# Optimization experiments

Hardware: AMD Instinct MI355X
Metric: run time of the kernel (lower is better)

The kernel has to match this reference:

```python
import jax, jax.numpy as jnp
import numpy as np

N = 1_000_000  # nodes
E = 1_000_000  # edges (== N so poss_edge can be indexed by node ids AND edge masks, as in source)
C = 64         # classes; poss_edge has C+1 columns (last = 'intrust')
SEMI_LAMBDA = 0.5
EDGE_LAMBDA = 1.0


def setup_inputs() -> dict:
    key = jax.random.key(0)
    k1, k2, k3, k4, k5 = jax.random.split(key, 5)
    # probabilities strictly positive so log() is finite
    poss_node = jax.random.uniform(k1, (N, C), jnp.float32, 0.05, 1.0)
    poss_edge = jax.random.uniform(k2, (E, C + 1), jnp.float32, 0.05, 1.0)
    groundTruth = jax.random.randint(k3, (N,), 0, C)
    mask = jax.random.randint(k4, (N,), 0, 2).astype(bool)
    edges = jax.random.randint(k5, (E, 2), 0, N)
    return {"poss_node": poss_node, "poss_edge": poss_edge,
            "groundTruth": groundTruth, "mask": mask, "edges": edges}


def reference(poss_node, poss_edge, groundTruth, mask, edges):
    dt = poss_node.dtype
    maskf = mask.astype(dt)
    # --- node NLL loss: mean of -log p[i, gt[i]] over masked nodes ---
    logp = jnp.log(poss_node[jnp.arange(N), groundTruth])  # [N]
    loss = -jnp.sum(maskf * logp) / jnp.sum(maskf)

    e0, e1 = edges[:, 0], edges[:, 1]
    intrust = jax.lax.stop_gradient(poss_edge[:, -1])  # detach

    # --- semi loss (faithful to source: scalar sq-diff times sum(1-intrust)) ---
    if SEMI_LAMBDA >= 1e-9:
        sqdiff = jnp.sum((poss_edge[e0] - poss_edge[e1]) ** 2)  # scalar
        semi_loss = SEMI_LAMBDA * jnp.sum(1.0 - intrust) * sqdiff
    else:
        semi_loss = jnp.zeros((), dt)

    # --- edge label splits ---
    m0, m1 = mask[e0], mask[e1]
    label_mask = m0 | m1
    both = m0 & m1
    gt0, gt1 = groundTruth[e0], groundTruth[e1]
    same = both & (gt0 == gt1)
    diff = both & (gt0 != gt1)
    single = label_mask & ~both
    left_s = single & m0
    right_s = single & m1

    rows = jnp.arange(E)
    p_gt0 = poss_edge[rows, gt0]   # [E] prob of left node's label
    p_gt1 = poss_edge[rows, gt1]   # [E] prob of right node's label
    p_last = poss_edge[:, -1]      # [E] 'no-edge' / intrust column

    z = jnp.zeros((), dt)
    raw = (-jnp.sum(jnp.where(same, jnp.log(p_gt0), z))
           - jnp.sum(jnp.where(diff, jnp.log(p_last), z))
           - jnp.sum(jnp.where(left_s, jnp.log(p_last + p_gt0), z))
           - jnp.sum(jnp.where(right_s, jnp.log(p_last + p_gt1), z)))
    S = jnp.sum(label_mask.astype(dt))
    # source applies (*= edge_lambda; /= S) twice
    edge_loss = raw * (EDGE_LAMBDA * EDGE_LAMBDA) / (S * S)

    return loss + semi_loss + edge_loss
```

## Files before the change

### kernel.cpp

```cpp
#include <hip/hip_runtime.h>
#include <math.h>

namespace {
constexpr int N = 1000000;
constexpr int E = 1000000;
constexpr int C = 64;
constexpr int NODE_BLOCKS = 1024;
constexpr int EDGE_BLOCKS = 2048;
constexpr int BLOCK = 256;
constexpr int GROUPS_PER_BLOCK = BLOCK / 16;
constexpr int TOTAL_GROUPS = EDGE_BLOCKS * GROUPS_PER_BLOCK;
constexpr double SEMI_LAMBDA = 0.5;
constexpr double EDGE_LAMBDA = 1.0;
}

__device__ __forceinline__ float waveReduceSum(float v) {
#pragma unroll
    for (int off = 32; off > 0; off >>= 1) v += __shfl_down(v, off, 64);
    return v;
}

__global__ __launch_bounds__(BLOCK) void node_kernel(
    const float* __restrict__ poss_node,
    const int* __restrict__ gt,
    const int* __restrict__ mask,
    float* __restrict__ partials)
{
    float lsum = 0.f, cnt = 0.f;
    for (int i = blockIdx.x * BLOCK + threadIdx.x; i < N; i += NODE_BLOCKS * BLOCK) {
        if (mask[i] != 0) {
            lsum += logf(poss_node[(size_t)i * C + gt[i]]);
            cnt += 1.f;
        }
    }
    __shared__ float s0[BLOCK / 64], s1[BLOCK / 64];
    lsum = waveReduceSum(lsum);
    cnt  = waveReduceSum(cnt);
    const int lane = threadIdx.x & 63, wv = threadIdx.x >> 6;
    if (lane == 0) { s0[wv] = lsum; s1[wv] = cnt; }
    __syncthreads();
    if (threadIdx.x == 0) {
        float a = 0.f, b = 0.f;
#pragma unroll
        for (int w = 0; w < BLOCK / 64; ++w) { a += s0[w]; b += s1[w]; }
        partials[blockIdx.x]               = a;
        partials[NODE_BLOCKS + blockIdx.x] = b;
    }
}

__global__ __launch_bounds__(BLOCK) void edge_kernel(
    const float* __restrict__ poss_edge,
    const int* __restrict__ gt,
    const int* __restrict__ mask,
    const int* __restrict__ edges,
    float* __restrict__ partials)
{
    const int t   = threadIdx.x & 15;
    const int grp = threadIdx.x >> 4;
    const int globalGroup = blockIdx.x * GROUPS_PER_BLOCK + grp;

    float s1 = 0.f, sq = 0.f, pos = 0.f, lcnt = 0.f;

    for (int e = globalGroup; e < E; e += TOTAL_GROUPS) {
        const int2 ep = *(const int2*)(edges + 2 * (size_t)e);
        const int e0 = ep.x, e1 = ep.y;

        const float* __restrict__ ra = poss_edge + (size_t)e0 * (C + 1);
        const float* __restrict__ rb = poss_edge + (size_t)e1 * (C + 1);
        const float* __restrict__ re = poss_edge + (size_t)e  * (C + 1);

        const float a0 = ra[t], a1 = ra[t + 16], a2 = ra[t + 32], a3 = ra[t + 48];
        const float b0 = rb[t], b1 = rb[t + 16], b2 = rb[t + 32], b3 = rb[t + 48];
        const float d0 = a0 - b0, d1 = a1 - b1, d2 = a2 - b2, d3 = a3 - b3;
        float acc = fmaf(d0, d0, fmaf(d1, d1, fmaf(d2, d2, d3 * d3)));
        if (t == 0) {
            const float dl = ra[C] - rb[C];
            acc = fmaf(dl, dl, acc);
        }
        sq += acc;

        const float p_last = re[C];
        const int m0 = (mask[e0] != 0);
        const int m1 = (mask[e1] != 0);
        if (m0 | m1) {
            const int g0 = gt[e0];
            const int g1 = gt[e1];
            float contrib;
            if (m0 & m1) {
                contrib = (g0 == g1) ? logf(re[g0]) : logf(p_last);
            } else if (m0) {
                contrib = logf(p_last + re[g0]);
            } else {
                contrib = logf(p_last + re[g1]);
            }
            if (t == 0) { pos += contrib; lcnt += 1.f; }
        }
        if (t == 0) s1 += 1.f - p_last;
    }

    __shared__ float s[4][BLOCK / 64];
    s1   = waveReduceSum(s1);
    sq   = waveReduceSum(sq);
    pos  = waveReduceSum(pos);
    lcnt = waveReduceSum(lcnt);
    const int lane = threadIdx.x & 63, wv = threadIdx.x >> 6;
    if (lane == 0) { s[0][wv] = s1; s[1][wv] = sq; s[2][wv] = pos; s[3][wv] = lcnt; }
    __syncthreads();
    if (threadIdx.x == 0) {
        float a = 0.f, b = 0.f, c = 0.f, d = 0.f;
#pragma unroll
        for (int w = 0; w < BLOCK / 64; ++w) {
            a += s[0][w]; b += s[1][w]; c += s[2][w]; d += s[3][w];
        }
        partials[0 * EDGE_BLOCKS + blockIdx.x] = a;
        partials[1 * EDGE_BLOCKS + blockIdx.x] = b;
        partials[2 * EDGE_BLOCKS + blockIdx.x] = c;
        partials[3 * EDGE_BLOCKS + blockIdx.x] = d;
    }
}

__global__ __launch_bounds__(BLOCK) void finalize_kernel(
    const float* __restrict__ node_partials,
    const float* __restrict__ edge_partials,
    float* __restrict__ out)
{
    double a0 = 0, a1 = 0, a2 = 0, a3 = 0, a4 = 0, a5 = 0;
    for (int i = threadIdx.x; i < NODE_BLOCKS; i += BLOCK) {
        a0 += (double)node_partials[i];
        a1 += (double)node_partials[NODE_BLOCKS + i];
    }
    for (int i = threadIdx.x; i < EDGE_BLOCKS; i += BLOCK) {
        a2 += (double)edge_partials[0 * EDGE_BLOCKS + i];
        a3 += (double)edge_partials[1 * EDGE_BLOCKS + i];
        a4 += (double)edge_partials[2 * EDGE_BLOCKS + i];
        a5 += (double)edge_partials[3 * EDGE_BLOCKS + i];
    }
#pragma unroll
    for (int off = 32; off > 0; off >>= 1) {
        a0 += __shfl_down(a0, off, 64);
        a1 += __shfl_down(a1, off, 64);
        a2 += __shfl_down(a2, off, 64);
        a3 += __shfl_down(a3, off, 64);
        a4 += __shfl_down(a4, off, 64);
        a5 += __shfl_down(a5, off, 64);
    }
    __shared__ double sd[6][BLOCK / 64];
    const int lane = threadIdx.x & 63, wv = threadIdx.x >> 6;
    if (lane == 0) {
        sd[0][wv] = a0; sd[1][wv] = a1; sd[2][wv] = a2;
        sd[3][wv] = a3; sd[4][wv] = a4; sd[5][wv] = a5;
    }
    __syncthreads();
    if (threadIdx.x == 0) {
        double t[6];
#pragma unroll
        for (int k = 0; k < 6; ++k) {
            double v = 0;
#pragma unroll
            for (int w = 0; w < BLOCK / 64; ++w) v += sd[k][w];
            t[k] = v;
        }
        const double logp_sum  = t[0];
        const double mask_cnt  = t[1];
        const double s1_sum    = t[2];
        const double sq_sum    = t[3];
        const double pos_sum   = t[4];
        const double label_cnt = t[5];

        const double loss      = -logp_sum / mask_cnt;
        const double semi      = SEMI_LAMBDA * s1_sum * sq_sum;
        const double raw       = -pos_sum;
        const double edge_loss = raw * (EDGE_LAMBDA * EDGE_LAMBDA) / (label_cnt * label_cnt);

        out[0] = (float)(loss + semi + edge_loss);
    }
}

extern "C" void kernel_launch(void* const* d_in, const int* in_sizes, int n_in,
                              void* d_out, int out_size, void* d_ws, size_t ws_size,
                              hipStream_t stream) {
    const float* poss_node = (const float*)d_in[0];
    const float* poss_edge = (const float*)d_in[1];
    const int*   gt        = (const int*)d_in[2];
    const int*   mask      = (const int*)d_in[3];
    const int*   edges     = (const int*)d_in[4];
    float*       out       = (float*)d_out;

    float* node_partials = (float*)d_ws;
    float* edge_partials = node_partials + 2 * NODE_BLOCKS;

    node_kernel<<<NODE_BLOCKS, BLOCK, 0, stream>>>(poss_node, gt, mask, node_partials);
    edge_kernel<<<EDGE_BLOCKS, BLOCK, 0, stream>>>(poss_edge, gt, mask, edges, edge_partials);
    finalize_kernel<<<1, BLOCK, 0, stream>>>(node_partials, edge_partials, out);
}
```

Baseline: 582.6 us.

## Convert poss_edge to packed fp16 table before random-gather edge pass

Adds a prep kernel that streams poss_edge once, writes a compact fp16 copy of the 64 class columns plus a separate fp32 last-column array, and computes the node loss in the same launch. The edge kernel then gathers 128-byte fp16 rows instead of unaligned 260-byte fp32 rows, aiming to cut random-gather traffic and make it cache friendlier. The cost is an extra full read and write pass over poss_edge, plus fp16 rounding of the squared-difference and label-probability terms. A fallback to the original path runs when the workspace is too small.

```diff
diff --git a/kernel.cpp b/kernel.cpp
--- a/kernel.cpp
+++ b/kernel.cpp
@@ -5,14 +5,29 @@
 constexpr int N = 1000000;
 constexpr int E = 1000000;
 constexpr int C = 64;
-constexpr int NODE_BLOCKS = 1024;
-constexpr int EDGE_BLOCKS = 2048;
 constexpr int BLOCK = 256;
 constexpr int GROUPS_PER_BLOCK = BLOCK / 16;
-constexpr int TOTAL_GROUPS = EDGE_BLOCKS * GROUPS_PER_BLOCK;
+
+constexpr int PREP_BLOCKS = 2048;
+constexpr int EDGE_BLOCKS = 2048;
+constexpr int PREP_GROUPS = PREP_BLOCKS * GROUPS_PER_BLOCK;
+constexpr int EDGE_GROUPS = EDGE_BLOCKS * GROUPS_PER_BLOCK;
+
+constexpr int NODE_BLOCKS_F = 1024;
+constexpr int EDGE_BLOCKS_F = 2048;
+constexpr int TOTAL_GROUPS_F = EDGE_BLOCKS_F * GROUPS_PER_BLOCK;
+
 constexpr double SEMI_LAMBDA = 0.5;
 constexpr double EDGE_LAMBDA = 1.0;
-}
+
+constexpr size_t PE16_ELEMS = (size_t)E * C;
+constexpr size_t WS_NEEDED  = PE16_ELEMS * 2
+                            + (size_t)E * 4
+                            + (size_t)3 * PREP_BLOCKS * 4
+                            + (size_t)3 * EDGE_BLOCKS * 4;
+}
+
+union H4 { uint2 u2; _Float16 h[4]; };
 
 __device__ __forceinline__ float waveReduceSum(float v) {
 #pragma unroll
@@ -20,14 +35,201 @@
     return v;
 }
 
-__global__ __launch_bounds__(BLOCK) void node_kernel(
+
+__device__ __forceinline__ void node_phase(const float* __restrict__ poss_node,
+                                           const int* __restrict__ gt,
+                                           const int* __restrict__ mask,
+                                           float& lsum, float& cnt) {
+    for (int i = blockIdx.x * BLOCK + threadIdx.x; i < N; i += PREP_BLOCKS * BLOCK) {
+        if (mask[i] != 0) {
+            lsum += logf(poss_node[(size_t)i * C + gt[i]]);
+            cnt += 1.f;
+        }
+    }
+}
+
+__device__ __forceinline__ void row_phase(const float* __restrict__ poss_edge,
+                                          unsigned short* __restrict__ pe16,
+                                          float* __restrict__ plast,
+                                          float& s1) {
+    const int t = threadIdx.x & 15;
+    const int g = blockIdx.x * GROUPS_PER_BLOCK + (threadIdx.x >> 4);
+    for (int r = g; r < E; r += PREP_GROUPS) {
+        const float* __restrict__ row = poss_edge + (size_t)r * (C + 1);
+        H4 h;
+        h.h[0] = (_Float16)row[4 * t + 0];
+        h.h[1] = (_Float16)row[4 * t + 1];
+        h.h[2] = (_Float16)row[4 * t + 2];
+        h.h[3] = (_Float16)row[4 * t + 3];
+        *reinterpret_cast<uint2*>(pe16 + (size_t)r * C + 4 * t) = h.u2;
+        if (t == 0) {
+            const float pl = row[C];
+            plast[r] = pl;
+            s1 += 1.f - pl;
+        }
+    }
+}
+
+__global__ __launch_bounds__(BLOCK) void prep_kernel(
+    const float* __restrict__ poss_node,
+    const float* __restrict__ poss_edge,
+    const int* __restrict__ gt,
+    const int* __restrict__ mask,
+    unsigned short* __restrict__ pe16,
+    float* __restrict__ plast,
+    float* __restrict__ partials)
+{
+    float lsum = 0.f, cnt = 0.f, s1 = 0.f;
+    if (blockIdx.x & 1) {
+        node_phase(poss_node, gt, mask, lsum, cnt);
+        row_phase(poss_edge, pe16, plast, s1);
+    } else {
+        row_phase(poss_edge, pe16, plast, s1);
+        node_phase(poss_node, gt, mask, lsum, cnt);
+    }
+
+    __shared__ float s[3][BLOCK / 64];
+    lsum = waveReduceSum(lsum);
+    cnt  = waveReduceSum(cnt);
+    s1   = waveReduceSum(s1);
+    const int lane = threadIdx.x & 63, wv = threadIdx.x >> 6;
+    if (lane == 0) { s[0][wv] = lsum; s[1][wv] = cnt; s[2][wv] = s1; }
+    __syncthreads();
+    if (threadIdx.x == 0) {
+        float a = 0.f, b = 0.f, c = 0.f;
+#pragma unroll
+        for (int w = 0; w < BLOCK / 64; ++w) { a += s[0][w]; b += s[1][w]; c += s[2][w]; }
+        partials[0 * PREP_BLOCKS + blockIdx.x] = a;
+        partials[1 * PREP_BLOCKS + blockIdx.x] = b;
+        partials[2 * PREP_BLOCKS + blockIdx.x] = c;
+    }
+}
+
+__global__ __launch_bounds__(BLOCK) void edge16_kernel(
+    const unsigned short* __restrict__ pe16,
+    const float* __restrict__ plast,
+    const int* __restrict__ gt,
+    const int* __restrict__ mask,
+    const int* __restrict__ edges,
+    float* __restrict__ partials)
+{
+    const int t = threadIdx.x & 15;
+    const int g = blockIdx.x * GROUPS_PER_BLOCK + (threadIdx.x >> 4);
+
+    float sq = 0.f, pos = 0.f, lcnt = 0.f;
+
+    for (int e = g; e < E; e += EDGE_GROUPS) {
+        const int2 ep = *(const int2*)(edges + 2 * (size_t)e);
+        const int e0 = ep.x, e1 = ep.y;
+
+        H4 ha, hb;
+        ha.u2 = *reinterpret_cast<const uint2*>(pe16 + (size_t)e0 * C + 4 * t);
+        hb.u2 = *reinterpret_cast<const uint2*>(pe16 + (size_t)e1 * C + 4 * t);
+        const float d0 = (float)ha.h[0] - (float)hb.h[0];
+        const float d1 = (float)ha.h[1] - (float)hb.h[1];
+        const float d2 = (float)ha.h[2] - (float)hb.h[2];
+        const float d3 = (float)ha.h[3] - (float)hb.h[3];
+        float acc = fmaf(d0, d0, fmaf(d1, d1, fmaf(d2, d2, d3 * d3)));
+        if (t == 0) {
+            const float dl = plast[e0] - plast[e1];
+            acc = fmaf(dl, dl, acc);
+        }
+        sq += acc;
+
+        const float p_last = plast[e];
+        const int m0 = (mask[e0] != 0);
+        const int m1 = (mask[e1] != 0);
+        if (m0 | m1) {
+            const int g0 = gt[e0];
+            const int g1 = gt[e1];
+            float contrib;
+            if (m0 & m1) {
+                contrib = (g0 == g1)
+                    ? logf((float)*reinterpret_cast<const _Float16*>(pe16 + (size_t)e * C + g0))
+                    : logf(p_last);
+            } else if (m0) {
+                contrib = logf(p_last + (float)*reinterpret_cast<const _Float16*>(pe16 + (size_t)e * C + g0));
+            } else {
+                contrib = logf(p_last + (float)*reinterpret_cast<const _Float16*>(pe16 + (size_t)e * C + g1));
+            }
+            if (t == 0) { pos += contrib; lcnt += 1.f; }
+        }
+    }
+
+    __shared__ float s[3][BLOCK / 64];
+    sq   = waveReduceSum(sq);
+    pos  = waveReduceSum(pos);
+    lcnt = waveReduceSum(lcnt);
+    const int lane = threadIdx.x & 63, wv = threadIdx.x >> 6;
+    if (lane == 0) { s[0][wv] = sq; s[1][wv] = pos; s[2][wv] = lcnt; }
+    __syncthreads();
+    if (threadIdx.x == 0) {
+        float a = 0.f, b = 0.f, c = 0.f;
+#pragma unroll
+        for (int w = 0; w < BLOCK / 64; ++w) { a += s[0][w]; b += s[1][w]; c += s[2][w]; }
+        partials[0 * EDGE_BLOCKS + blockIdx.x] = a;
+        partials[1 * EDGE_BLOCKS + blockIdx.x] = b;
+        partials[2 * EDGE_BLOCKS + blockIdx.x] = c;
+    }
+}
+
+__global__ __launch_bounds__(BLOCK) void finalize16_kernel(
+    const float* __restrict__ prep_partials,
+    const float* __restrict__ edge_partials,
+    float* __restrict__ out)
+{
+    double a0 = 0, a1 = 0, a2 = 0, a3 = 0, a4 = 0, a5 = 0;
+    for (int i = threadIdx.x; i < PREP_BLOCKS; i += BLOCK) {
+        a0 += (double)prep_partials[0 * PREP_BLOCKS + i];
+        a1 += (double)prep_partials[1 * PREP_BLOCKS + i];
+        a2 += (double)prep_partials[2 * PREP_BLOCKS + i];
+    }
+    for (int i = threadIdx.x; i < EDGE_BLOCKS; i += BLOCK) {
+        a3 += (double)edge_partials[0 * EDGE_BLOCKS + i];
+        a4 += (double)edge_partials[1 * EDGE_BLOCKS + i];
+        a5 += (double)edge_partials[2 * EDGE_BLOCKS + i];
+    }
+#pragma unroll
+    for (int off = 32; off > 0; off >>= 1) {
+        a0 += __shfl_down(a0, off, 64);
+        a1 += __shfl_down(a1, off, 64);
+        a2 += __shfl_down(a2, off, 64);
+        a3 += __shfl_down(a3, off, 64);
+        a4 += __shfl_down(a4, off, 64);
+        a5 += __shfl_down(a5, off, 64);
+    }
+    __shared__ double sd[6][BLOCK / 64];
+    const int lane = threadIdx.x & 63, wv = threadIdx.x >> 6;
+    if (lane == 0) {
+        sd[0][wv] = a0; sd[1][wv] = a1; sd[2][wv] = a2;
+        sd[3][wv] = a3; sd[4][wv] = a4; sd[5][wv] = a5;
+    }
+    __syncthreads();
+    if (threadIdx.x == 0) {
+        double t[6];
+#pragma unroll
+        for (int k = 0; k < 6; ++k) {
+            double v = 0;
+#pragma unroll
+            for (int w = 0; w < BLOCK / 64; ++w) v += sd[k][w];
+            t[k] = v;
+        }
+        const double loss      = -t[0] / t[1];
+        const double semi      = SEMI_LAMBDA * t[2] * t[3];
+        const double edge_loss = (-t[4]) * (EDGE_LAMBDA * EDGE_LAMBDA) / (t[5] * t[5]);
+        out[0] = (float)(loss + semi + edge_loss);
+    }
+}
+
+
+__global__ __launch_bounds__(BLOCK) void node_kernel_f(
     const float* __restrict__ poss_node,
     const int* __restrict__ gt,
     const int* __restrict__ mask,
     float* __restrict__ partials)
 {
     float lsum = 0.f, cnt = 0.f;
-    for (int i = blockIdx.x * BLOCK + threadIdx.x; i < N; i += NODE_BLOCKS * BLOCK) {
+    for (int i = blockIdx.x * BLOCK + threadIdx.x; i < N; i += NODE_BLOCKS_F * BLOCK) {
         if (mask[i] != 0) {
             lsum += logf(poss_node[(size_t)i * C + gt[i]]);
             cnt += 1.f;
@@ -43,12 +245,12 @@
         float a = 0.f, b = 0.f;
 #pragma unroll
         for (int w = 0; w < BLOCK / 64; ++w) { a += s0[w]; b += s1[w]; }
-        partials[blockIdx.x]               = a;
-        partials[NODE_BLOCKS + blockIdx.x] = b;
-    }
-}
-
-__global__ __launch_bounds__(BLOCK) void edge_kernel(
+        partials[blockIdx.x]                 = a;
+        partials[NODE_BLOCKS_F + blockIdx.x] = b;
+    }
+}
+
+__global__ __launch_bounds__(BLOCK) void edge_kernel_f(
     const float* __restrict__ poss_edge,
     const int* __restrict__ gt,
     const int* __restrict__ mask,
@@ -61,7 +263,7 @@
 
     float s1 = 0.f, sq = 0.f, pos = 0.f, lcnt = 0.f;
 
-    for (int e = globalGroup; e < E; e += TOTAL_GROUPS) {
+    for (int e = globalGroup; e < E; e += TOTAL_GROUPS_F) {
         const int2 ep = *(const int2*)(edges + 2 * (size_t)e);
         const int e0 = ep.x, e1 = ep.y;
 
@@ -112,28 +314,28 @@
         for (int w = 0; w < BLOCK / 64; ++w) {
             a += s[0][w]; b += s[1][w]; c += s[2][w]; d += s[3][w];
         }
-        partials[0 * EDGE_BLOCKS + blockIdx.x] = a;
-        partials[1 * EDGE_BLOCKS + blockIdx.x] = b;
-        partials[2 * EDGE_BLOCKS + blockIdx.x] = c;
-        partials[3 * EDGE_BLOCKS + blockIdx.x] = d;
-    }
-}
-
-__global__ __launch_bounds__(BLOCK) void finalize_kernel(
+        partials[0 * EDGE_BLOCKS_F + blockIdx.x] = a;
+        partials[1 * EDGE_BLOCKS_F + blockIdx.x] = b;
+        partials[2 * EDGE_BLOCKS_F + blockIdx.x] = c;
+        partials[3 * EDGE_BLOCKS_F + blockIdx.x] = d;
+    }
+}
+
+__global__ __launch_bounds__(BLOCK) void finalize_kernel_f(
     const float* __restrict__ node_partials,
     const float* __restrict__ edge_partials,
     float* __restrict__ out)
 {
     double a0 = 0, a1 = 0, a2 = 0, a3 = 0, a4 = 0, a5 = 0;
-    for (int i = threadIdx.x; i < NODE_BLOCKS; i += BLOCK) {
+    for (int i = threadIdx.x; i < NODE_BLOCKS_F; i += BLOCK) {
         a0 += (double)node_partials[i];
-        a1 += (double)node_partials[NODE_BLOCKS + i];
-    }
-    for (int i = threadIdx.x; i < EDGE_BLOCKS; i += BLOCK) {
-        a2 += (double)edge_partials[0 * EDGE_BLOCKS + i];
-        a3 += (double)edge_partials[1 * EDGE_BLOCKS + i];
-        a4 += (double)edge_partials[2 * EDGE_BLOCKS + i];
-        a5 += (double)edge_partials[3 * EDGE_BLOCKS + i];
+        a1 += (double)node_partials[NODE_BLOCKS_F + i];
+    }
+    for (int i = threadIdx.x; i < EDGE_BLOCKS_F; i += BLOCK) {
+        a2 += (double)edge_partials[0 * EDGE_BLOCKS_F + i];
+        a3 += (double)edge_partials[1 * EDGE_BLOCKS_F + i];
+        a4 += (double)edge_partials[2 * EDGE_BLOCKS_F + i];
+        a5 += (double)edge_partials[3 * EDGE_BLOCKS_F + i];
     }
 #pragma unroll
     for (int off = 32; off > 0; off >>= 1) {
@@ -160,21 +362,13 @@
             for (int w = 0; w < BLOCK / 64; ++w) v += sd[k][w];
             t[k] = v;
         }
-        const double logp_sum  = t[0];
-        const double mask_cnt  = t[1];
-        const double s1_sum    = t[2];
-        const double sq_sum    = t[3];
-        const double pos_sum   = t[4];
-        const double label_cnt = t[5];
-
-        const double loss      = -logp_sum / mask_cnt;
-        const double semi      = SEMI_LAMBDA * s1_sum * sq_sum;
-        const double raw       = -pos_sum;
-        const double edge_loss = raw * (EDGE_LAMBDA * EDGE_LAMBDA) / (label_cnt * label_cnt);
-
+        const double loss      = -t[0] / t[1];
+        const double semi      = SEMI_LAMBDA * t[2] * t[3];
+        const double edge_loss = (-t[4]) * (EDGE_LAMBDA * EDGE_LAMBDA) / (t[5] * t[5]);
         out[0] = (float)(loss + semi + edge_loss);
     }
 }
+
 
 extern "C" void kernel_launch(void* const* d_in, const int* in_sizes, int n_in,
                               void* d_out, int out_size, void* d_ws, size_t ws_size,
@@ -186,10 +380,23 @@
     const int*   edges     = (const int*)d_in[4];
     float*       out       = (float*)d_out;
 
-    float* node_partials = (float*)d_ws;
-    float* edge_partials = node_partials + 2 * NODE_BLOCKS;
-
-    node_kernel<<<NODE_BLOCKS, BLOCK, 0, stream>>>(poss_node, gt, mask, node_partials);
-    edge_kernel<<<EDGE_BLOCKS, BLOCK, 0, stream>>>(poss_edge, gt, mask, edges, edge_partials);
-    finalize_kernel<<<1, BLOCK, 0, stream>>>(node_partials, edge_partials, out);
-}
+    if (ws_size >= WS_NEEDED) {
+        unsigned short* pe16          = (unsigned short*)d_ws;
+        float*          plast         = (float*)(pe16 + PE16_ELEMS);
+        float*          prep_partials = plast + E;
+        float*          edge_partials = prep_partials + 3 * PREP_BLOCKS;
+
+        prep_kernel<<<PREP_BLOCKS, BLOCK, 0, stream>>>(
+            poss_node, poss_edge, gt, mask, pe16, plast, prep_partials);
+        edge16_kernel<<<EDGE_BLOCKS, BLOCK, 0, stream>>>(
+            pe16, plast, gt, mask, edges, edge_partials);
+        finalize16_kernel<<<1, BLOCK, 0, stream>>>(prep_partials, edge_partials, out);
+    } else {
+        float* node_partials = (float*)d_ws;
+        float* edge_partials = node_partials + 2 * NODE_BLOCKS_F;
+
+        node_kernel_f<<<NODE_BLOCKS_F, BLOCK, 0, stream>>>(poss_node, gt, mask, node_partials);
+        edge_kernel_f<<<EDGE_BLOCKS_F, BLOCK, 0, stream>>>(poss_edge, gt, mask, edges, edge_partials);
+        finalize_kernel_f<<<1, BLOCK, 0, stream>>>(node_partials, edge_partials, out);
+    }
+}
```

Result: slower. 613.2 us (+5.3%).
